# Kernel tuning notes

Measured on AMD Instinct MI355X. Metric: run time of the kernel, lower is better.

Reference implementation:

```python
import jax, jax.numpy as jnp
import numpy as np

TOKENS, D_MODEL, N_EXPERTS, K = 16384, 4096, 64, 2


def setup_inputs() -> dict:
    key = jax.random.key(0)
    kx, kw, kb = jax.random.split(key, 3)
    x = jax.random.normal(kx, (TOKENS, D_MODEL), dtype=jnp.float32)
    # nn.Linear(input_dim, num_experts): weight [num_experts, input_dim], bias [num_experts]
    bound = 1.0 / np.sqrt(D_MODEL)
    W = jax.random.uniform(kw, (N_EXPERTS, D_MODEL), minval=-bound, maxval=bound, dtype=jnp.float32)
    b = jax.random.uniform(kb, (N_EXPERTS,), minval=-bound, maxval=bound, dtype=jnp.float32)
    return {"x": x, "W": W, "b": b}


def reference(x, W, b):
    # logits = x @ W.T + b ; softmax over experts ; top-k
    logits = jnp.einsum('td,ed->te', x, W) + b  # [tokens, experts]
    scores = jax.nn.softmax(logits, axis=-1)
    topk_scores, topk_indices = jax.lax.top_k(scores, K)
    return (topk_indices, topk_scores)
```

## Files before the change

kernel.cpp:

```cpp
#include <hip/hip_runtime.h>
#include <hip/hip_bf16.h>
#include <cstdint>
#include <cstddef>

#define TOKENS 16384
#define DMODEL 4096
#define NEXP   64
#define NWAVE  4
#define KSPAN  (DMODEL / NWAVE)
#define NKC    (KSPAN / 16)

typedef __attribute__((ext_vector_type(8)))  short bf16x8;
typedef __attribute__((ext_vector_type(16))) float f32x16;

__device__ __forceinline__ void cvt_hilo8(const float f[8], bf16x8* hi, bf16x8* lo) {
  union { __hip_bfloat16 b; unsigned short u; } cv;
  bf16x8 hv, lv;
#pragma unroll
  for (int j = 0; j < 8; ++j) {
    __hip_bfloat16 hb = __float2bfloat16(f[j]);
    cv.b = hb; hv[j] = (short)cv.u;
    float r = f[j] - __bfloat162float(hb);
    cv.b = __float2bfloat16(r); lv[j] = (short)cv.u;
  }
  *hi = hv; *lo = lv;
}

__global__ __launch_bounds__(256)
void prep_W(const float* __restrict__ W, uint4* __restrict__ wh, uint4* __restrict__ wl) {
  const int tid = blockIdx.x * 256 + threadIdx.x;
  const int l  = tid & 63;
  const int et = (tid >> 6) & 1;
  const int kc = tid >> 7;
  const int e  = et * 32 + (l & 31);
  const int k  = kc * 16 + (l >> 5) * 8;
  const float* src = W + (size_t)e * DMODEL + k;
  float f[8];
#pragma unroll
  for (int j = 0; j < 8; ++j) f[j] = src[j];
  bf16x8 hi, lo;
  cvt_hilo8(f, &hi, &lo);
  const int slot = (kc * 2 + et) * 64 + l;
  wh[slot] = __builtin_bit_cast(uint4, hi);
  wl[slot] = __builtin_bit_cast(uint4, lo);
}

__global__ __launch_bounds__(256, 2)
void gemm_topk(const float* __restrict__ x, const uint4* __restrict__ wh,
               const uint4* __restrict__ wl, const float* __restrict__ b,
               float* __restrict__ out) {
  __shared__ float red[NWAVE][32 * NEXP];

  const int tid = threadIdx.x;
  const int l   = tid & 63;
  const int w   = tid >> 6;
  const int t0  = blockIdx.x * 32;
  const int row = l & 31, g = l >> 5;

  const float* xp  = x  + (size_t)(t0 + row) * DMODEL + w * KSPAN + g * 8;
  const uint4* whp = wh + (size_t)w * (NKC * 128) + l;
  const uint4* wlp = wl + (size_t)w * (NKC * 128) + l;

  f32x16 acc0, acc1;
#pragma unroll
  for (int i = 0; i < 16; ++i) { acc0[i] = 0.f; acc1[i] = 0.f; }

  float4 a0 = *(const float4*)(xp);
  float4 a1 = *(const float4*)(xp + 4);
  uint4 bh0 = whp[0], bh1 = whp[64];
  uint4 bl0 = wlp[0], bl1 = wlp[64];

  for (int kc = 0; kc < NKC; ++kc) {
    float4 na0 = a0, na1 = a1; uint4 nh0 = bh0, nh1 = bh1, nl0 = bl0, nl1 = bl1;
    if (kc + 1 < NKC) {
      const float* xn = xp + (kc + 1) * 16;
      na0 = *(const float4*)(xn);
      na1 = *(const float4*)(xn + 4);
      const uint4* whn = whp + (kc + 1) * 128;
      const uint4* wln = wlp + (kc + 1) * 128;
      nh0 = whn[0]; nh1 = whn[64];
      nl0 = wln[0]; nl1 = wln[64];
    }
    float f[8] = {a0.x, a0.y, a0.z, a0.w, a1.x, a1.y, a1.z, a1.w};
    bf16x8 ah, al;
    cvt_hilo8(f, &ah, &al);
    bf16x8 vh0 = __builtin_bit_cast(bf16x8, bh0);
    bf16x8 vh1 = __builtin_bit_cast(bf16x8, bh1);
    bf16x8 vl0 = __builtin_bit_cast(bf16x8, bl0);
    bf16x8 vl1 = __builtin_bit_cast(bf16x8, bl1);
    acc0 = __builtin_amdgcn_mfma_f32_32x32x16_bf16(ah, vh0, acc0, 0, 0, 0);
    acc1 = __builtin_amdgcn_mfma_f32_32x32x16_bf16(ah, vh1, acc1, 0, 0, 0);
    acc0 = __builtin_amdgcn_mfma_f32_32x32x16_bf16(ah, vl0, acc0, 0, 0, 0);
    acc1 = __builtin_amdgcn_mfma_f32_32x32x16_bf16(ah, vl1, acc1, 0, 0, 0);
    acc0 = __builtin_amdgcn_mfma_f32_32x32x16_bf16(al, vh0, acc0, 0, 0, 0);
    acc1 = __builtin_amdgcn_mfma_f32_32x32x16_bf16(al, vh1, acc1, 0, 0, 0);
    a0 = na0; a1 = na1; bh0 = nh0; bh1 = nh1; bl0 = nl0; bl1 = nl1;
  }

  {
    float* rp = &red[w][0];
#pragma unroll
    for (int r = 0; r < 16; ++r) {
      const int rr = (r & 3) + 8 * (r >> 2) + 4 * g;
      rp[rr * NEXP + row]      = acc0[r];
      rp[rr * NEXP + 32 + row] = acc1[r];
    }
  }
  __syncthreads();

  const float bias = b[tid & 63];
#pragma unroll
  for (int j = 0; j < 8; ++j) {
    const int f = tid + 256 * j;
    float s = red[0][f] + red[1][f] + red[2][f] + red[3][f] + bias;
    red[0][f] = s;
  }
  __syncthreads();

#pragma unroll
  for (int i = 0; i < 8; ++i) {
    const int tl = w * 8 + i;
    const float v = red[0][tl * NEXP + l];

    float m1 = v; int i1 = l;
#pragma unroll
    for (int off = 32; off > 0; off >>= 1) {
      float ov = __shfl_xor(m1, off, 64);
      int   oi = __shfl_xor(i1, off, 64);
      if (ov > m1 || (ov == m1 && oi < i1)) { m1 = ov; i1 = oi; }
    }
    float v2 = (l == i1) ? -__builtin_inff() : v;
    float m2 = v2; int i2 = l;
#pragma unroll
    for (int off = 32; off > 0; off >>= 1) {
      float ov = __shfl_xor(m2, off, 64);
      int   oi = __shfl_xor(i2, off, 64);
      if (ov > m2 || (ov == m2 && oi < i2)) { m2 = ov; i2 = oi; }
    }
    float e = __expf(v - m1);
#pragma unroll
    for (int off = 32; off > 0; off >>= 1) e += __shfl_xor(e, off, 64);

    if (l == 0) {
      const int t = t0 + tl;
      out[(size_t)t * 2 + 0] = (float)i1;
      out[(size_t)t * 2 + 1] = (float)i2;
      float inv = 1.0f / e;
      out[(size_t)TOKENS * 2 + (size_t)t * 2 + 0] = inv;
      out[(size_t)TOKENS * 2 + (size_t)t * 2 + 1] = __expf(m2 - m1) * inv;
    }
  }
}

extern "C" void kernel_launch(void* const* d_in, const int* in_sizes, int n_in,
                              void* d_out, int out_size, void* d_ws, size_t ws_size,
                              hipStream_t stream) {
  const float* x = (const float*)d_in[0];
  const float* W = (const float*)d_in[1];
  const float* b = (const float*)d_in[2];
  float* out = (float*)d_out;

  uint4* wh = (uint4*)d_ws;
  uint4* wl = wh + 32768;

  hipLaunchKernelGGL(prep_W,    dim3(128),        dim3(256), 0, stream, W, wh, wl);
  hipLaunchKernelGGL(gemm_topk, dim3(TOKENS / 32), dim3(256), 0, stream, x, wh, wl, b, out);
}
```

Baseline: 83.14 us.

## Split the K dimension across eight waves and double-buffer register prefetch

Each block now runs eight waves instead of four. Each wave covers half as much of the model dimension, and the partial logits are reduced across eight LDS slices. The global loads of x and the pre-split weights are prefetched two K-chunks ahead using a two-slot register ring, which hides more memory latency. The cost is double the LDS per block, more reduction work, and a launch bound of (512, 4) that may squeeze the register budget enough to cause spills.

```diff
diff --git a/kernel.cpp b/kernel.cpp
--- a/kernel.cpp
+++ b/kernel.cpp
@@ -6,7 +6,7 @@
 #define TOKENS 16384
 #define DMODEL 4096
 #define NEXP   64
-#define NWAVE  4
+#define NWAVE  8
 #define KSPAN  (DMODEL / NWAVE)
 #define NKC    (KSPAN / 16)
 
@@ -45,7 +45,7 @@
   wl[slot] = __builtin_bit_cast(uint4, lo);
 }
 
-__global__ __launch_bounds__(256, 2)
+__global__ __launch_bounds__(512, 4)
 void gemm_topk(const float* __restrict__ x, const uint4* __restrict__ wh,
                const uint4* __restrict__ wl, const float* __restrict__ b,
                float* __restrict__ out) {
@@ -65,22 +65,26 @@
 #pragma unroll
   for (int i = 0; i < 16; ++i) { acc0[i] = 0.f; acc1[i] = 0.f; }
 
-  float4 a0 = *(const float4*)(xp);
-  float4 a1 = *(const float4*)(xp + 4);
-  uint4 bh0 = whp[0], bh1 = whp[64];
-  uint4 bl0 = wlp[0], bl1 = wlp[64];
+  float4 px0[2], px1[2];
+  uint4  ph0[2], ph1[2], pl0[2], pl1[2];
 
-  for (int kc = 0; kc < NKC; ++kc) {
-    float4 na0 = a0, na1 = a1; uint4 nh0 = bh0, nh1 = bh1, nl0 = bl0, nl1 = bl1;
-    if (kc + 1 < NKC) {
-      const float* xn = xp + (kc + 1) * 16;
-      na0 = *(const float4*)(xn);
-      na1 = *(const float4*)(xn + 4);
-      const uint4* whn = whp + (kc + 1) * 128;
-      const uint4* wln = wlp + (kc + 1) * 128;
-      nh0 = whn[0]; nh1 = whn[64];
-      nl0 = wln[0]; nl1 = wln[64];
-    }
+  auto ldx = [&](int kc, int s) {
+    const float* xn = xp + kc * 16;
+    px0[s] = *(const float4*)(xn);
+    px1[s] = *(const float4*)(xn + 4);
+  };
+  auto ldw = [&](int kc, int s) {
+    ph0[s] = whp[kc * 128];  ph1[s] = whp[kc * 128 + 64];
+    pl0[s] = wlp[kc * 128];  pl1[s] = wlp[kc * 128 + 64];
+  };
+
+  ldx(0, 0); ldw(0, 0);
+  ldx(1, 1); ldw(1, 1);
+
+  auto step = [&](int kc, int s) {
+    float4 a0 = px0[s], a1 = px1[s];
+    uint4 bh0 = ph0[s], bh1 = ph1[s], bl0 = pl0[s], bl1 = pl1[s];
+    if (kc + 2 < NKC) { ldx(kc + 2, s); ldw(kc + 2, s); }
     float f[8] = {a0.x, a0.y, a0.z, a0.w, a1.x, a1.y, a1.z, a1.w};
     bf16x8 ah, al;
     cvt_hilo8(f, &ah, &al);
@@ -94,8 +98,9 @@
     acc1 = __builtin_amdgcn_mfma_f32_32x32x16_bf16(ah, vl1, acc1, 0, 0, 0);
     acc0 = __builtin_amdgcn_mfma_f32_32x32x16_bf16(al, vh0, acc0, 0, 0, 0);
     acc1 = __builtin_amdgcn_mfma_f32_32x32x16_bf16(al, vh1, acc1, 0, 0, 0);
-    a0 = na0; a1 = na1; bh0 = nh0; bh1 = nh1; bl0 = nl0; bl1 = nl1;
-  }
+  };
+
+  for (int kc = 0; kc < NKC; kc += 2) { step(kc, 0); step(kc + 1, 1); }
 
   {
     float* rp = &red[w][0];
@@ -110,16 +115,17 @@
 
   const float bias = b[tid & 63];
 #pragma unroll
-  for (int j = 0; j < 8; ++j) {
-    const int f = tid + 256 * j;
-    float s = red[0][f] + red[1][f] + red[2][f] + red[3][f] + bias;
+  for (int j = 0; j < 4; ++j) {
+    const int f = tid + 512 * j;
+    float s = red[0][f] + red[1][f] + red[2][f] + red[3][f]
+            + red[4][f] + red[5][f] + red[6][f] + red[7][f] + bias;
     red[0][f] = s;
   }
   __syncthreads();
 
 #pragma unroll
-  for (int i = 0; i < 8; ++i) {
-    const int tl = w * 8 + i;
+  for (int i = 0; i < 4; ++i) {
+    const int tl = w * 4 + i;
     const float v = red[0][tl * NEXP + l];
 
     float m1 = v; int i1 = l;
@@ -163,6 +169,6 @@
   uint4* wh = (uint4*)d_ws;
   uint4* wl = wh + 32768;
 
-  hipLaunchKernelGGL(prep_W,    dim3(128),        dim3(256), 0, stream, W, wh, wl);
-  hipLaunchKernelGGL(gemm_topk, dim3(TOKENS / 32), dim3(256), 0, stream, x, wh, wl, b, out);
+  hipLaunchKernelGGL(prep_W,    dim3(128),         dim3(256), 0, stream, W, wh, wl);
+  hipLaunchKernelGGL(gemm_topk, dim3(TOKENS / 32), dim3(512), 0, stream, x, wh, wl, b, out);
 }
```

After: 82.24 us. About the same (-1.1%).

## Stage x through double-buffered swizzled LDS and split experts across waves

Applied to the files above, without the earlier changes.

Switches the GEMM from splitting K across four waves to splitting the 64 experts across waves. Each wave now uses 16x16x32 MFMAs with its own W slice. x is loaded cooperatively in 256-column windows, converted once to bf16 hi/lo, and written into double-buffered XOR-swizzled LDS that all waves share. This removes the cross-wave K reduction, so the x hi/lo conversion is done once per element rather than being tied to each wave's K span. The cost is two barriers per window and the full 64KB of LDS, which may limit occupancy to one block per CU.

```diff
diff --git a/kernel.cpp b/kernel.cpp
--- a/kernel.cpp
+++ b/kernel.cpp
@@ -6,12 +6,12 @@
 #define TOKENS 16384
 #define DMODEL 4096
 #define NEXP   64
-#define NWAVE  4
-#define KSPAN  (DMODEL / NWAVE)
-#define NKC    (KSPAN / 16)
-
-typedef __attribute__((ext_vector_type(8)))  short bf16x8;
-typedef __attribute__((ext_vector_type(16))) float f32x16;
+#define NWIN   16
+#define WINK   256
+#define NKC2   128
+
+typedef __attribute__((ext_vector_type(8))) short bf16x8;
+typedef __attribute__((ext_vector_type(4))) float f32x4;
 
 __device__ __forceinline__ void cvt_hilo8(const float f[8], bf16x8* hi, bf16x8* lo) {
   union { __hip_bfloat16 b; unsigned short u; } cv;
@@ -29,98 +29,135 @@
 __global__ __launch_bounds__(256)
 void prep_W(const float* __restrict__ W, uint4* __restrict__ wh, uint4* __restrict__ wl) {
   const int tid = blockIdx.x * 256 + threadIdx.x;
-  const int l  = tid & 63;
-  const int et = (tid >> 6) & 1;
-  const int kc = tid >> 7;
-  const int e  = et * 32 + (l & 31);
-  const int k  = kc * 16 + (l >> 5) * 8;
+  const int l   = tid & 63;
+  const int eg  = (tid >> 6) & 3;
+  const int kc2 = tid >> 8;
+  const int e   = eg * 16 + (l & 15);
+  const int k   = kc2 * 32 + (l >> 4) * 8;
   const float* src = W + (size_t)e * DMODEL + k;
   float f[8];
 #pragma unroll
   for (int j = 0; j < 8; ++j) f[j] = src[j];
   bf16x8 hi, lo;
   cvt_hilo8(f, &hi, &lo);
-  const int slot = (kc * 2 + et) * 64 + l;
+  const int slot = (kc2 * 4 + eg) * 64 + l;
   wh[slot] = __builtin_bit_cast(uint4, hi);
   wl[slot] = __builtin_bit_cast(uint4, lo);
 }
 
+__device__ __forceinline__ int xaddr(int s) {
+  return (s * 16) ^ (((s >> 7) & 7) << 4);
+}
+
+__device__ __forceinline__ void loadx4(const float* __restrict__ x, int t0, int w, int l,
+                                       int win, float4 L[8]) {
+#pragma unroll
+  for (int j = 0; j < 4; ++j) {
+    const float* p = x + (size_t)(t0 + w * 8 + 2 * j + (l >> 5)) * DMODEL
+                       + win * WINK + (l & 31) * 8;
+    L[j * 2]     = *(const float4*)p;
+    L[j * 2 + 1] = *(const float4*)(p + 4);
+  }
+}
+
+__device__ __forceinline__ void cvtwrite(char* hb, char* lb, int w, int l,
+                                         const float4 L[8]) {
+  const int kc2l = (l & 31) >> 2;
+  const int ksub = l & 3;
+  const int mt   = w >> 1;
+#pragma unroll
+  for (int j = 0; j < 4; ++j) {
+    const int r  = w * 8 + 2 * j + (l >> 5);
+    const int lp = (r & 15) + ksub * 16;
+    const int a  = xaddr((kc2l * 2 + mt) * 64 + lp);
+    float f[8] = {L[j*2].x, L[j*2].y, L[j*2].z, L[j*2].w,
+                  L[j*2+1].x, L[j*2+1].y, L[j*2+1].z, L[j*2+1].w};
+    bf16x8 hi, lo;
+    cvt_hilo8(f, &hi, &lo);
+    *(bf16x8*)(hb + a) = hi;
+    *(bf16x8*)(lb + a) = lo;
+  }
+}
+
+__device__ __forceinline__ void compute_win(const char* hb, const char* lb, int wi, int l,
+    const uint4* __restrict__ whp, const uint4* __restrict__ wlp,
+    uint4 (&ph)[2], uint4 (&pl)[2], f32x4& acc0, f32x4& acc1) {
+#pragma unroll
+  for (int c = 0; c < 8; ++c) {
+    uint4 bhu = ph[c & 1], blu = pl[c & 1];
+    const int kci = wi * 8 + c;
+    if (kci + 2 < NKC2) {
+      ph[c & 1] = whp[(kci + 2) * 256];
+      pl[c & 1] = wlp[(kci + 2) * 256];
+    }
+    const int s0 = (c * 2 + 0) * 64 + l;
+    const int s1 = (c * 2 + 1) * 64 + l;
+    bf16x8 ah0 = *(const bf16x8*)(hb + xaddr(s0));
+    bf16x8 ah1 = *(const bf16x8*)(hb + xaddr(s1));
+    bf16x8 al0 = *(const bf16x8*)(lb + xaddr(s0));
+    bf16x8 al1 = *(const bf16x8*)(lb + xaddr(s1));
+    bf16x8 bh = __builtin_bit_cast(bf16x8, bhu);
+    bf16x8 bl = __builtin_bit_cast(bf16x8, blu);
+    acc0 = __builtin_amdgcn_mfma_f32_16x16x32_bf16(ah0, bh, acc0, 0, 0, 0);
+    acc1 = __builtin_amdgcn_mfma_f32_16x16x32_bf16(ah1, bh, acc1, 0, 0, 0);
+    acc0 = __builtin_amdgcn_mfma_f32_16x16x32_bf16(ah0, bl, acc0, 0, 0, 0);
+    acc1 = __builtin_amdgcn_mfma_f32_16x16x32_bf16(ah1, bl, acc1, 0, 0, 0);
+    acc0 = __builtin_amdgcn_mfma_f32_16x16x32_bf16(al0, bh, acc0, 0, 0, 0);
+    acc1 = __builtin_amdgcn_mfma_f32_16x16x32_bf16(al1, bh, acc1, 0, 0, 0);
+  }
+}
+
 __global__ __launch_bounds__(256, 2)
-void gemm_topk(const float* __restrict__ x, const uint4* __restrict__ wh,
-               const uint4* __restrict__ wl, const float* __restrict__ b,
+void gemm_topk(const float* __restrict__ x, const uint4* __restrict__ whB,
+               const uint4* __restrict__ wlB, const float* __restrict__ b,
                float* __restrict__ out) {
-  __shared__ float red[NWAVE][32 * NEXP];
-
+  __shared__ __align__(16) char lds[65536];
   const int tid = threadIdx.x;
   const int l   = tid & 63;
   const int w   = tid >> 6;
   const int t0  = blockIdx.x * 32;
-  const int row = l & 31, g = l >> 5;
-
-  const float* xp  = x  + (size_t)(t0 + row) * DMODEL + w * KSPAN + g * 8;
-  const uint4* whp = wh + (size_t)w * (NKC * 128) + l;
-  const uint4* wlp = wl + (size_t)w * (NKC * 128) + l;
-
-  f32x16 acc0, acc1;
-#pragma unroll
-  for (int i = 0; i < 16; ++i) { acc0[i] = 0.f; acc1[i] = 0.f; }
-
-  float4 a0 = *(const float4*)(xp);
-  float4 a1 = *(const float4*)(xp + 4);
-  uint4 bh0 = whp[0], bh1 = whp[64];
-  uint4 bl0 = wlp[0], bl1 = wlp[64];
-
-  for (int kc = 0; kc < NKC; ++kc) {
-    float4 na0 = a0, na1 = a1; uint4 nh0 = bh0, nh1 = bh1, nl0 = bl0, nl1 = bl1;
-    if (kc + 1 < NKC) {
-      const float* xn = xp + (kc + 1) * 16;
-      na0 = *(const float4*)(xn);
-      na1 = *(const float4*)(xn + 4);
-      const uint4* whn = whp + (kc + 1) * 128;
-      const uint4* wln = wlp + (kc + 1) * 128;
-      nh0 = whn[0]; nh1 = whn[64];
-      nl0 = wln[0]; nl1 = wln[64];
-    }
-    float f[8] = {a0.x, a0.y, a0.z, a0.w, a1.x, a1.y, a1.z, a1.w};
-    bf16x8 ah, al;
-    cvt_hilo8(f, &ah, &al);
-    bf16x8 vh0 = __builtin_bit_cast(bf16x8, bh0);
-    bf16x8 vh1 = __builtin_bit_cast(bf16x8, bh1);
-    bf16x8 vl0 = __builtin_bit_cast(bf16x8, bl0);
-    bf16x8 vl1 = __builtin_bit_cast(bf16x8, bl1);
-    acc0 = __builtin_amdgcn_mfma_f32_32x32x16_bf16(ah, vh0, acc0, 0, 0, 0);
-    acc1 = __builtin_amdgcn_mfma_f32_32x32x16_bf16(ah, vh1, acc1, 0, 0, 0);
-    acc0 = __builtin_amdgcn_mfma_f32_32x32x16_bf16(ah, vl0, acc0, 0, 0, 0);
-    acc1 = __builtin_amdgcn_mfma_f32_32x32x16_bf16(ah, vl1, acc1, 0, 0, 0);
-    acc0 = __builtin_amdgcn_mfma_f32_32x32x16_bf16(al, vh0, acc0, 0, 0, 0);
-    acc1 = __builtin_amdgcn_mfma_f32_32x32x16_bf16(al, vh1, acc1, 0, 0, 0);
-    a0 = na0; a1 = na1; bh0 = nh0; bh1 = nh1; bl0 = nl0; bl1 = nl1;
-  }
-
-  {
-    float* rp = &red[w][0];
-#pragma unroll
-    for (int r = 0; r < 16; ++r) {
-      const int rr = (r & 3) + 8 * (r >> 2) + 4 * g;
-      rp[rr * NEXP + row]      = acc0[r];
-      rp[rr * NEXP + 32 + row] = acc1[r];
-    }
-  }
+
+  char* h0 = lds;              char* l0 = lds + 16384;
+  char* h1 = lds + 32768;      char* l1 = lds + 49152;
+  const uint4* whp = whB + w * 64 + l;
+  const uint4* wlp = wlB + w * 64 + l;
+
+  f32x4 acc0 = {0.f, 0.f, 0.f, 0.f}, acc1 = {0.f, 0.f, 0.f, 0.f};
+  float4 LR0[8], LR1[8];
+
+  loadx4(x, t0, w, l, 0, LR0);
+  cvtwrite(h0, l0, w, l, LR0);
+  loadx4(x, t0, w, l, 1, LR1);
+  uint4 ph[2], pl[2];
+  ph[0] = whp[0];   pl[0] = wlp[0];
+  ph[1] = whp[256]; pl[1] = wlp[256];
   __syncthreads();
 
-  const float bias = b[tid & 63];
-#pragma unroll
-  for (int j = 0; j < 8; ++j) {
-    const int f = tid + 256 * j;
-    float s = red[0][f] + red[1][f] + red[2][f] + red[3][f] + bias;
-    red[0][f] = s;
+  for (int wi = 0; wi < NWIN; wi += 2) {
+    if (wi + 2 < NWIN) loadx4(x, t0, w, l, wi + 2, LR0);
+    cvtwrite(h1, l1, w, l, LR1);
+    compute_win(h0, l0, wi, l, whp, wlp, ph, pl, acc0, acc1);
+    __syncthreads();
+    if (wi + 3 < NWIN) loadx4(x, t0, w, l, wi + 3, LR1);
+    if (wi + 2 < NWIN) cvtwrite(h0, l0, w, l, LR0);
+    compute_win(h1, l1, wi + 1, l, whp, wlp, ph, pl, acc0, acc1);
+    __syncthreads();
+  }
+
+  float* red = (float*)lds;
+  const float bias = b[w * 16 + (l & 15)];
+#pragma unroll
+  for (int reg = 0; reg < 4; ++reg) {
+    const int tr = (l >> 4) * 4 + reg;
+    red[tr * 66 + w * 16 + (l & 15)]        = acc0[reg] + bias;
+    red[(16 + tr) * 66 + w * 16 + (l & 15)] = acc1[reg] + bias;
   }
   __syncthreads();
 
 #pragma unroll
   for (int i = 0; i < 8; ++i) {
     const int tl = w * 8 + i;
-    const float v = red[0][tl * NEXP + l];
+    const float v = red[tl * 66 + l];
 
     float m1 = v; int i1 = l;
 #pragma unroll
@@ -163,6 +200,6 @@
   uint4* wh = (uint4*)d_ws;
   uint4* wl = wh + 32768;
 
-  hipLaunchKernelGGL(prep_W,    dim3(128),        dim3(256), 0, stream, W, wh, wl);
+  hipLaunchKernelGGL(prep_W,    dim3(128),         dim3(256), 0, stream, W, wh, wl);
   hipLaunchKernelGGL(gemm_topk, dim3(TOKENS / 32), dim3(256), 0, stream, x, wh, wl, b, out);
 }
```

Measured after the change: 85.94 us. +3.4%, slower.
